# Kernel optimization log

Hardware: AMD Instinct MI355X
Metric: run time of the kernel (lower is better)

## Reference

```python
import jax, jax.numpy as jnp
import numpy as np

N_EXPERTS = 8
D_IN = 1024
D_OUT = 1024
BATCH = 4096


def setup_inputs() -> dict:
    key = jax.random.key(0)
    k_x, k_w, k_b, k_a = jax.random.split(key, 4)
    xs = jax.random.normal(k_x, (BATCH, D_IN), dtype=jnp.float32)
    mxs = jnp.arange(BATCH, dtype=jnp.int32)  # opaque per-sample metadata, passed through
    actions = jax.random.randint(k_a, (BATCH,), 0, N_EXPERTS, dtype=jnp.int64)
    # Expert parameters: each submodule is Linear(D_IN -> D_OUT)
    W = jax.random.normal(k_w, (N_EXPERTS, D_OUT, D_IN), dtype=jnp.float32) / np.sqrt(D_IN)
    b = jax.random.normal(k_b, (N_EXPERTS, D_OUT), dtype=jnp.float32) * 0.01
    return {"xs": xs, "mxs": mxs, "actions": actions, "W": W, "b": b}


def reference(xs, mxs, actions, W, b):
    # Original: per-sample python loop y_i = submodule[actions[i]](x_i); cat along batch.
    # Vectorized: compute all experts densely (E small), then select per-sample row.
    y_all = jnp.einsum("bj,eij->bei", xs, W) + b[None, :, :]  # [B, E, D_OUT]
    ys = jnp.take_along_axis(y_all, actions[:, None, None].astype(jnp.int32), axis=1)
    ys = jnp.squeeze(ys, axis=1)  # [B, D_OUT]
    return (ys, mxs, actions)
```

## Files before the change

kernel.cpp:

```cpp
#include <hip/hip_runtime.h>

#define BATCH 4096
#define D_IN 1024
#define D_OUT 1024
#define N_EXPERTS 8

#define TM 64
#define TN 128
#define TK 32
#define MAX_TILES 71

#define WS_PERM    0
#define WS_STARTS  4096
#define WS_TILE_E  4112
#define WS_TILE_M  4200
#define WS_NTILES  4288

typedef __attribute__((ext_vector_type(8))) short short8;
typedef __attribute__((ext_vector_type(4))) float f32x4;

__global__ void group_kernel(const int* __restrict__ actions, int* __restrict__ ws) {
    __shared__ int cnt[N_EXPERTS];
    __shared__ int base[N_EXPERTS];
    const int t = threadIdx.x;
    if (t < N_EXPERTS) cnt[t] = 0;
    __syncthreads();
    for (int i = t; i < BATCH; i += 256) atomicAdd(&cnt[actions[i]], 1);
    __syncthreads();
    if (t == 0) {
        int s = 0, nt = 0;
        for (int e = 0; e < N_EXPERTS; ++e) {
            const int c = cnt[e];
            base[e] = s;
            ws[WS_STARTS + e] = s;
            for (int m0 = 0; m0 < c; m0 += TM) {
                ws[WS_TILE_E + nt] = e;
                ws[WS_TILE_M + nt] = m0;
                ++nt;
            }
            s += c;
            cnt[e] = 0;
        }
        ws[WS_STARTS + N_EXPERTS] = s;
        ws[WS_NTILES] = nt;
    }
    __syncthreads();
    for (int i = t; i < BATCH; i += 256) {
        const int a = actions[i];
        const int pos = base[a] + atomicAdd(&cnt[a], 1);
        ws[WS_PERM + pos] = i;
    }
}

__device__ __forceinline__ void cvt8(const float4 a, const float4 b,
                                     short8& h, short8& l) {
    float f[8] = {a.x, a.y, a.z, a.w, b.x, b.y, b.z, b.w};
#pragma unroll
    for (int i = 0; i < 8; ++i) {
        const unsigned u = __float_as_uint(f[i]);
        h[i] = (short)(u >> 16);
        const float r = f[i] - __uint_as_float(u & 0xffff0000u);
        l[i] = (short)(__float_as_uint(r) >> 16);
    }
}

__global__ __launch_bounds__(256) void moe_gemm(
    const float* __restrict__ xs, const float* __restrict__ W,
    const float* __restrict__ bias, const int* __restrict__ ws,
    float* __restrict__ out)
{
    const int tix = blockIdx.y;
    if (tix >= ws[WS_NTILES]) return;
    const int e   = ws[WS_TILE_E + tix];
    const int m0  = ws[WS_TILE_M + tix];
    const int s0  = ws[WS_STARTS + e];
    const int cnt = ws[WS_STARTS + e + 1] - s0;
    const int n0  = blockIdx.x * TN;

    __shared__ short Ahi[2][TM * TK];
    __shared__ short Alo[2][TM * TK];
    __shared__ short Bhi[2][TN * TK];
    __shared__ short Blo[2][TN * TK];
    __shared__ int   rows_s[TM];

    const int t = threadIdx.x;
    if (t < TM) {
        const int r = m0 + t;
        rows_s[t] = (r < cnt) ? ws[WS_PERM + s0 + r] : -1;
    }
    __syncthreads();

    const int lane = t & 63;
    const int wave = t >> 6;
    const int wm = (wave & 1) * 32;
    const int wn = (wave >> 1) * 64;

    const float zf = 0.f;
    f32x4 acc[2][4];
#pragma unroll
    for (int mi = 0; mi < 2; ++mi)
#pragma unroll
        for (int nj = 0; nj < 4; ++nj)
            acc[mi][nj] = (f32x4){zf, zf, zf, zf};

    const float* Wb = W + (size_t)e * (D_OUT * (size_t)D_IN) + (size_t)n0 * D_IN;

    const int j  = t & 3;
    const int rr = t >> 2;

    const int arow = rows_s[rr];
    const float* aptr = (arow >= 0) ? (xs + (size_t)arow * D_IN + j * 8) : nullptr;

    const int slotA   = (j * 16 + (rr & 15)) ^ (j << 1);
    const int aoff_st = (rr >> 4) * 512 + slotA * 8;
    const int boff0   = aoff_st;
    const int boff1   = aoff_st + 4 * 512;

    const float* qb0 = Wb + (size_t)rr * D_IN + j * 8;
    const float* qb1 = Wb + (size_t)(64 + rr) * D_IN + j * 8;

    const int rds = (lane ^ ((lane >> 4) << 1)) * 8;

#define LOAD_SET(A0, A1, B0, B1, B2, B3, KOFF) do {                          \
        const int _k = (KOFF);                                               \
        if (aptr) {                                                          \
            A0 = *(const float4*)(aptr + _k);                                \
            A1 = *(const float4*)(aptr + _k + 4);                            \
        }                                                                    \
        B0 = *(const float4*)(qb0 + _k); B1 = *(const float4*)(qb0 + _k + 4);\
        B2 = *(const float4*)(qb1 + _k); B3 = *(const float4*)(qb1 + _k + 4);\
    } while (0)

#define CVT_STORE_SET(A0, A1, B0, B1, B2, B3, BUF) do {                      \
        short8 _h, _l;                                                       \
        cvt8(A0, A1, _h, _l);                                                \
        *(short8*)&Ahi[BUF][aoff_st] = _h; *(short8*)&Alo[BUF][aoff_st] = _l;\
        cvt8(B0, B1, _h, _l);                                                \
        *(short8*)&Bhi[BUF][boff0] = _h;   *(short8*)&Blo[BUF][boff0] = _l;  \
        cvt8(B2, B3, _h, _l);                                                \
        *(short8*)&Bhi[BUF][boff1] = _h;   *(short8*)&Blo[BUF][boff1] = _l;  \
    } while (0)

#define FRAG_MFMA(BUF) do {                                                  \
        short8 ah[2], al[2], bh[4], bl[4];                                   \
        _Pragma("unroll")                                                    \
        for (int i2 = 0; i2 < 2; ++i2) {                                     \
            const int aoff = ((wm >> 4) + i2) * 512 + rds;                   \
            ah[i2] = *(const short8*)&Ahi[BUF][aoff];                        \
            al[i2] = *(const short8*)&Alo[BUF][aoff];                        \
        }                                                                    \
        _Pragma("unroll")                                                    \
        for (int i2 = 0; i2 < 4; ++i2) {                                     \
            const int boff = ((wn >> 4) + i2) * 512 + rds;                   \
            bh[i2] = *(const short8*)&Bhi[BUF][boff];                        \
            bl[i2] = *(const short8*)&Blo[BUF][boff];                        \
        }                                                                    \
        _Pragma("unroll")                                                    \
        for (int mi = 0; mi < 2; ++mi)                                       \
            _Pragma("unroll")                                                \
            for (int nj = 0; nj < 4; ++nj) {                                 \
                acc[mi][nj] = __builtin_amdgcn_mfma_f32_16x16x32_bf16(ah[mi], bh[nj], acc[mi][nj], 0, 0, 0); \
                acc[mi][nj] = __builtin_amdgcn_mfma_f32_16x16x32_bf16(ah[mi], bl[nj], acc[mi][nj], 0, 0, 0); \
                acc[mi][nj] = __builtin_amdgcn_mfma_f32_16x16x32_bf16(al[mi], bh[nj], acc[mi][nj], 0, 0, 0); \
            }                                                                \
    } while (0)

#define PIPE_BARRIER() asm volatile("s_waitcnt lgkmcnt(0)\n\ts_barrier" ::: "memory")

    float4 ax0 = make_float4(0.f, 0.f, 0.f, 0.f), ax1 = ax0;
    float4 bx0, bx1, bx2, bx3;
    float4 ay0 = make_float4(0.f, 0.f, 0.f, 0.f), ay1 = ay0;
    float4 by0, by1, by2, by3;

    LOAD_SET(ax0, ax1, bx0, bx1, bx2, bx3, 0);
    CVT_STORE_SET(ax0, ax1, bx0, bx1, bx2, bx3, 0);
    LOAD_SET(ax0, ax1, bx0, bx1, bx2, bx3, TK);
    PIPE_BARRIER();

    int ke = 2 * TK;
#pragma unroll 1
    for (int i = 0; i < 15; ++i) {
        {
            LOAD_SET(ay0, ay1, by0, by1, by2, by3, ke);
            FRAG_MFMA(0);
            CVT_STORE_SET(ax0, ax1, bx0, bx1, bx2, bx3, 1);
            PIPE_BARRIER();
        }
        {
            LOAD_SET(ax0, ax1, bx0, bx1, bx2, bx3, ke + TK);
            FRAG_MFMA(1);
            CVT_STORE_SET(ay0, ay1, by0, by1, by2, by3, 0);
            PIPE_BARRIER();
        }
        ke += 2 * TK;
    }
    {
        FRAG_MFMA(0);
        CVT_STORE_SET(ax0, ax1, bx0, bx1, bx2, bx3, 1);
        PIPE_BARRIER();
    }
    {
        FRAG_MFMA(1);
    }

#undef LOAD_SET
#undef CVT_STORE_SET
#undef FRAG_MFMA
#undef PIPE_BARRIER

    const int cl = lane & 15;
    const int qd = lane >> 4;
    float bv[4];
#pragma unroll
    for (int nj = 0; nj < 4; ++nj)
        bv[nj] = bias[e * D_OUT + n0 + wn + nj * 16 + cl];
#pragma unroll
    for (int mi = 0; mi < 2; ++mi) {
#pragma unroll
        for (int reg = 0; reg < 4; ++reg) {
            const int mloc = wm + mi * 16 + qd * 4 + reg;
            const int r = rows_s[mloc];
            if (r >= 0) {
                float* orow = out + (size_t)r * D_OUT + n0 + wn + cl;
#pragma unroll
                for (int nj = 0; nj < 4; ++nj)
                    orow[nj * 16] = acc[mi][nj][reg] + bv[nj];
            }
        }
    }
}

__global__ void meta_float_kernel(const int* __restrict__ mxs,
                                  const int* __restrict__ actions,
                                  float* __restrict__ out) {
    const int i = blockIdx.x * 256 + threadIdx.x;
    if (i < BATCH) {
        out[BATCH * D_OUT + i] = (float)mxs[i];
        out[BATCH * D_OUT + BATCH + i] = (float)actions[i];
    }
}

__global__ void meta_raw64_kernel(const int* __restrict__ mxs,
                                  const int* __restrict__ actions,
                                  float* __restrict__ out) {
    const int i = blockIdx.x * 256 + threadIdx.x;
    if (i < BATCH) {
        out[BATCH * D_OUT + i] = (float)mxs[i];
        long long* a64 = (long long*)(out + BATCH * D_OUT + BATCH);
        a64[i] = (long long)actions[i];
    }
}

extern "C" void kernel_launch(void* const* d_in, const int* in_sizes, int n_in,
                              void* d_out, int out_size, void* d_ws, size_t ws_size,
                              hipStream_t stream) {
    const float* xs      = (const float*)d_in[0];
    const int*   mxs     = (const int*)d_in[1];
    const int*   actions = (const int*)d_in[2];
    const float* W       = (const float*)d_in[3];
    const float* bias    = (const float*)d_in[4];
    float* out = (float*)d_out;
    int*   ws  = (int*)d_ws;

    group_kernel<<<1, 256, 0, stream>>>(actions, ws);

    dim3 grid(D_OUT / TN, MAX_TILES, 1);
    moe_gemm<<<grid, 256, 0, stream>>>(xs, W, bias, ws, out);

    const int metaOff = BATCH * D_OUT;
    if (out_size >= metaOff + 3 * BATCH) {
        meta_raw64_kernel<<<(BATCH + 255) / 256, 256, 0, stream>>>(mxs, actions, out);
    } else if (out_size >= metaOff + 2 * BATCH) {
        meta_float_kernel<<<(BATCH + 255) / 256, 256, 0, stream>>>(mxs, actions, out);
    }
}
```

Baseline: 141.7 us.

## Pre-split inputs to bf16 hi/lo in workspace and stream tiles via global_load_lds

A new prep kernel converts all of xs and W into pre-tiled bf16 hi/lo arrays in the workspace. The same kernel also builds the expert grouping with a ballot-based parallel scan and writes the metadata outputs, replacing three separate kernels. The GEMM then loads these pre-converted tiles straight into LDS with global_load_lds, so the main loop no longer does fp32 loads and conversions. The cost is an extra full pass over W and xs every call, plus about 100MB of workspace traffic, with a fallback to the old GEMM when the workspace is too small.

```diff
diff --git a/kernel.cpp b/kernel.cpp
--- a/kernel.cpp
+++ b/kernel.cpp
@@ -16,41 +16,14 @@
 #define WS_TILE_M  4200
 #define WS_NTILES  4288
 
+#define WS_XHI_OFF   32768
+#define WS_XLO_OFF   (32768 + 8388608)
+#define WS_WHI_OFF   (32768 + 2*8388608)
+#define WS_WLO_OFF   (32768 + 2*8388608 + 16777216)
+#define WS_NEEDED    (32768 + 2*8388608 + 2*16777216)
+
 typedef __attribute__((ext_vector_type(8))) short short8;
 typedef __attribute__((ext_vector_type(4))) float f32x4;
-
-__global__ void group_kernel(const int* __restrict__ actions, int* __restrict__ ws) {
-    __shared__ int cnt[N_EXPERTS];
-    __shared__ int base[N_EXPERTS];
-    const int t = threadIdx.x;
-    if (t < N_EXPERTS) cnt[t] = 0;
-    __syncthreads();
-    for (int i = t; i < BATCH; i += 256) atomicAdd(&cnt[actions[i]], 1);
-    __syncthreads();
-    if (t == 0) {
-        int s = 0, nt = 0;
-        for (int e = 0; e < N_EXPERTS; ++e) {
-            const int c = cnt[e];
-            base[e] = s;
-            ws[WS_STARTS + e] = s;
-            for (int m0 = 0; m0 < c; m0 += TM) {
-                ws[WS_TILE_E + nt] = e;
-                ws[WS_TILE_M + nt] = m0;
-                ++nt;
-            }
-            s += c;
-            cnt[e] = 0;
-        }
-        ws[WS_STARTS + N_EXPERTS] = s;
-        ws[WS_NTILES] = nt;
-    }
-    __syncthreads();
-    for (int i = t; i < BATCH; i += 256) {
-        const int a = actions[i];
-        const int pos = base[a] + atomicAdd(&cnt[a], 1);
-        ws[WS_PERM + pos] = i;
-    }
-}
 
 __device__ __forceinline__ void cvt8(const float4 a, const float4 b,
                                      short8& h, short8& l) {
@@ -64,8 +37,148 @@
     }
 }
 
-__global__ __launch_bounds__(256) void moe_gemm(
+__global__ __launch_bounds__(256) void prep_kernel(
+    const int* __restrict__ actions, const int* __restrict__ mxs,
     const float* __restrict__ xs, const float* __restrict__ W,
+    int* __restrict__ ws,
+    short* __restrict__ XhiP, short* __restrict__ XloP,
+    short* __restrict__ WhiP, short* __restrict__ WloP,
+    float* __restrict__ out, int meta_mode)
+{
+    const int bid = blockIdx.x;
+    const int t = threadIdx.x;
+
+    if (bid == 0) {
+        __shared__ int chunkoff[64][N_EXPERTS];
+        const int lane = t & 63;
+        const int wave = t >> 6;
+
+        for (int it = 0; it < 16; ++it) {
+            const int c = wave * 16 + it;
+            const int a = actions[c * 64 + lane];
+            int myc = 0;
+#pragma unroll
+            for (int e = 0; e < N_EXPERTS; ++e) {
+                const unsigned long long me = __ballot(a == e);
+                if (lane == e) myc = (int)__popcll(me);
+            }
+            if (lane < N_EXPERTS) chunkoff[c][lane] = myc;
+        }
+        __syncthreads();
+
+        if (wave == 0) {
+            int cc0 = chunkoff[lane][0], cc1 = chunkoff[lane][1];
+            int cc2 = chunkoff[lane][2], cc3 = chunkoff[lane][3];
+            int cc4 = chunkoff[lane][4], cc5 = chunkoff[lane][5];
+            int cc6 = chunkoff[lane][6], cc7 = chunkoff[lane][7];
+            int tot0, tot1, tot2, tot3, tot4, tot5, tot6, tot7;
+            int ex0, ex1, ex2, ex3, ex4, ex5, ex6, ex7;
+#define SCAN1(CC, TOT, EX) do {                                   \
+            int v = CC;                                           \
+            _Pragma("unroll")                                     \
+            for (int d = 1; d < 64; d <<= 1) {                    \
+                const int u = __shfl_up(v, d, 64);                \
+                if (lane >= d) v += u;                            \
+            }                                                     \
+            TOT = __shfl(v, 63, 64);                              \
+            EX = v - CC;                                          \
+        } while (0)
+            SCAN1(cc0, tot0, ex0); SCAN1(cc1, tot1, ex1);
+            SCAN1(cc2, tot2, ex2); SCAN1(cc3, tot3, ex3);
+            SCAN1(cc4, tot4, ex4); SCAN1(cc5, tot5, ex5);
+            SCAN1(cc6, tot6, ex6); SCAN1(cc7, tot7, ex7);
+#undef SCAN1
+            const int b0 = 0;
+            const int b1 = b0 + tot0, b2 = b1 + tot1, b3 = b2 + tot2;
+            const int b4 = b3 + tot3, b5 = b4 + tot4, b6 = b5 + tot5;
+            const int b7 = b6 + tot6;
+            chunkoff[lane][0] = b0 + ex0; chunkoff[lane][1] = b1 + ex1;
+            chunkoff[lane][2] = b2 + ex2; chunkoff[lane][3] = b3 + ex3;
+            chunkoff[lane][4] = b4 + ex4; chunkoff[lane][5] = b5 + ex5;
+            chunkoff[lane][6] = b6 + ex6; chunkoff[lane][7] = b7 + ex7;
+            if (lane == 0) {
+                ws[WS_STARTS + 0] = b0; ws[WS_STARTS + 1] = b1;
+                ws[WS_STARTS + 2] = b2; ws[WS_STARTS + 3] = b3;
+                ws[WS_STARTS + 4] = b4; ws[WS_STARTS + 5] = b5;
+                ws[WS_STARTS + 6] = b6; ws[WS_STARTS + 7] = b7;
+                ws[WS_STARTS + 8] = BATCH;
+                int nt = 0;
+                int tots[8] = {tot0, tot1, tot2, tot3, tot4, tot5, tot6, tot7};
+#pragma unroll
+                for (int e = 0; e < N_EXPERTS; ++e)
+                    for (int m0 = 0; m0 < tots[e]; m0 += TM) {
+                        ws[WS_TILE_E + nt] = e;
+                        ws[WS_TILE_M + nt] = m0;
+                        ++nt;
+                    }
+                ws[WS_NTILES] = nt;
+            }
+        }
+        __syncthreads();
+
+        for (int it = 0; it < 16; ++it) {
+            const int c = wave * 16 + it;
+            const int i = c * 64 + lane;
+            const int a = actions[i];
+            unsigned long long msel = 0;
+#pragma unroll
+            for (int e = 0; e < N_EXPERTS; ++e) {
+                const unsigned long long me = __ballot(a == e);
+                if (a == e) msel = me;
+            }
+            const int rank = (int)__popcll(msel & ((1ull << lane) - 1ull));
+            const int pos = chunkoff[c][a] + rank;
+            ws[WS_PERM + pos] = i;
+        }
+        return;
+    }
+
+    if (bid <= 16) {
+        const int i = (bid - 1) * 256 + t;
+        if (meta_mode == 2) {
+            out[BATCH * D_OUT + i] = (float)mxs[i];
+            long long* a64 = (long long*)(out + BATCH * D_OUT + BATCH);
+            a64[i] = (long long)actions[i];
+        } else if (meta_mode == 1) {
+            out[BATCH * D_OUT + i] = (float)mxs[i];
+            out[BATCH * D_OUT + BATCH + i] = (float)actions[i];
+        }
+        return;
+    }
+
+    const int g = (bid - 17) * 256 + t;
+    if (g < 1048576) {
+        const int slot = g & 63;
+        const int i2   = (g >> 6) & 7;
+        const int blk  = g >> 9;
+        const int nt   = blk & 7;
+        const int kt   = (blk >> 3) & 31;
+        const int e    = blk >> 8;
+        const int c    = slot & 15;
+        const int j    = slot >> 4;
+        const int n    = nt * 128 + i2 * 16 + c;
+        const float* p = W + ((size_t)(e << 10) + n) * D_IN + kt * 32 + j * 8;
+        const float4 f0 = *(const float4*)p;
+        const float4 f1 = *(const float4*)(p + 4);
+        short8 h, l;
+        cvt8(f0, f1, h, l);
+        *(short8*)(WhiP + (size_t)g * 8) = h;
+        *(short8*)(WloP + (size_t)g * 8) = l;
+    } else {
+        const int g2 = g - 1048576;
+        const float* p = xs + (size_t)g2 * 8;
+        const float4 f0 = *(const float4*)p;
+        const float4 f1 = *(const float4*)(p + 4);
+        short8 h, l;
+        cvt8(f0, f1, h, l);
+        *(short8*)(XhiP + (size_t)g2 * 8) = h;
+        *(short8*)(XloP + (size_t)g2 * 8) = l;
+    }
+}
+
+__global__ __launch_bounds__(256) void moe_gemm_pc(
+    const short* __restrict__ Xhi, const short* __restrict__ Xlo,
+    const short* __restrict__ Whi, const short* __restrict__ Wlo,
     const float* __restrict__ bias, const int* __restrict__ ws,
     float* __restrict__ out)
 {
@@ -77,10 +190,10 @@
     const int cnt = ws[WS_STARTS + e + 1] - s0;
     const int n0  = blockIdx.x * TN;
 
-    __shared__ short Ahi[2][TM * TK];
-    __shared__ short Alo[2][TM * TK];
-    __shared__ short Bhi[2][TN * TK];
-    __shared__ short Blo[2][TN * TK];
+    __shared__ short Ahi[2][4 * 512];
+    __shared__ short Alo[2][4 * 512];
+    __shared__ short Bhi[2][8 * 512];
+    __shared__ short Blo[2][8 * 512];
     __shared__ int   rows_s[TM];
 
     const int t = threadIdx.x;
@@ -88,6 +201,13 @@
         const int r = m0 + t;
         rows_s[t] = (r < cnt) ? ws[WS_PERM + s0 + r] : -1;
     }
+    {
+        const short8 z = {0, 0, 0, 0, 0, 0, 0, 0};
+        ((short8*)&Ahi[0][0])[t] = z;
+        ((short8*)&Ahi[1][0])[t] = z;
+        ((short8*)&Alo[0][0])[t] = z;
+        ((short8*)&Alo[1][0])[t] = z;
+    }
     __syncthreads();
 
     const int lane = t & 63;
@@ -103,43 +223,49 @@
         for (int nj = 0; nj < 4; ++nj)
             acc[mi][nj] = (f32x4){zf, zf, zf, zf};
 
-    const float* Wb = W + (size_t)e * (D_OUT * (size_t)D_IN) + (size_t)n0 * D_IN;
-
-    const int j  = t & 3;
-    const int rr = t >> 2;
-
-    const int arow = rows_s[rr];
-    const float* aptr = (arow >= 0) ? (xs + (size_t)arow * D_IN + j * 8) : nullptr;
-
-    const int slotA   = (j * 16 + (rr & 15)) ^ (j << 1);
-    const int aoff_st = (rr >> 4) * 512 + slotA * 8;
-    const int boff0   = aoff_st;
-    const int boff1   = aoff_st + 4 * 512;
-
-    const float* qb0 = Wb + (size_t)rr * D_IN + j * 8;
-    const float* qb1 = Wb + (size_t)(64 + rr) * D_IN + j * 8;
-
-    const int rds = (lane ^ ((lane >> 4) << 1)) * 8;
-
-#define LOAD_SET(A0, A1, B0, B1, B2, B3, KOFF) do {                          \
-        const int _k = (KOFF);                                               \
-        if (aptr) {                                                          \
-            A0 = *(const float4*)(aptr + _k);                                \
-            A1 = *(const float4*)(aptr + _k + 4);                            \
-        }                                                                    \
-        B0 = *(const float4*)(qb0 + _k); B1 = *(const float4*)(qb0 + _k + 4);\
-        B2 = *(const float4*)(qb1 + _k); B3 = *(const float4*)(qb1 + _k + 4);\
+    const int arow = rows_s[wave * 16 + (lane & 15)];
+    const bool avalid = arow >= 0;
+    const short* aSrcHi = Xhi + (size_t)(avalid ? arow : 0) * D_IN + (lane >> 4) * 8;
+    const short* aSrcLo = Xlo + (size_t)(avalid ? arow : 0) * D_IN + (lane >> 4) * 8;
+
+    const size_t wBase = ((size_t)e * 256 + (size_t)blockIdx.x) * 4096;
+    const size_t bo0 = (size_t)wave * 512 + lane * 8;
+    const size_t bo1 = (size_t)(wave + 4) * 512 + lane * 8;
+
+#define STAGE(KT, BUF) do {                                                    \
+        const int _kt = (KT);                                                  \
+        if (avalid) {                                                          \
+            __builtin_amdgcn_global_load_lds(                                  \
+                (const __attribute__((address_space(1))) void*)(aSrcHi + _kt * 32), \
+                (__attribute__((address_space(3))) void*)&Ahi[BUF][wave * 512],\
+                16, 0, 0);                                                     \
+            __builtin_amdgcn_global_load_lds(                                  \
+                (const __attribute__((address_space(1))) void*)(aSrcLo + _kt * 32), \
+                (__attribute__((address_space(3))) void*)&Alo[BUF][wave * 512],\
+                16, 0, 0);                                                     \
+        }                                                                      \
+        {                                                                      \
+            const size_t _wo = wBase + (size_t)_kt * 32768;                    \
+            __builtin_amdgcn_global_load_lds(                                  \
+                (const __attribute__((address_space(1))) void*)(Whi + _wo + bo0), \
+                (__attribute__((address_space(3))) void*)&Bhi[BUF][wave * 512],\
+                16, 0, 0);                                                     \
+            __builtin_amdgcn_global_load_lds(                                  \
+                (const __attribute__((address_space(1))) void*)(Wlo + _wo + bo0), \
+                (__attribute__((address_space(3))) void*)&Blo[BUF][wave * 512],\
+                16, 0, 0);                                                     \
+            __builtin_amdgcn_global_load_lds(                                  \
+                (const __attribute__((address_space(1))) void*)(Whi + _wo + bo1), \
+                (__attribute__((address_space(3))) void*)&Bhi[BUF][(wave + 4) * 512], \
+                16, 0, 0);                                                     \
+            __builtin_amdgcn_global_load_lds(                                  \
+                (const __attribute__((address_space(1))) void*)(Wlo + _wo + bo1), \
+                (__attribute__((address_space(3))) void*)&Blo[BUF][(wave + 4) * 512], \
+                16, 0, 0);                                                     \
+        }                                                                      \
     } while (0)
 
-#define CVT_STORE_SET(A0, A1, B0, B1, B2, B3, BUF) do {                      \
-        short8 _h, _l;                                                       \
-        cvt8(A0, A1, _h, _l);                                                \
-        *(short8*)&Ahi[BUF][aoff_st] = _h; *(short8*)&Alo[BUF][aoff_st] = _l;\
-        cvt8(B0, B1, _h, _l);                                                \
-        *(short8*)&Bhi[BUF][boff0] = _h;   *(short8*)&Blo[BUF][boff0] = _l;  \
-        cvt8(B2, B3, _h, _l);                                                \
-        *(short8*)&Bhi[BUF][boff1] = _h;   *(short8*)&Blo[BUF][boff1] = _l;  \
-    } while (0)
+    const int rds = lane * 8;
 
 #define FRAG_MFMA(BUF) do {                                                  \
         short8 ah[2], al[2], bh[4], bl[4];                                   \
@@ -165,6 +291,154 @@
             }                                                                \
     } while (0)
 
+#define VBAR() asm volatile("s_waitcnt vmcnt(0) lgkmcnt(0)\n\ts_barrier" ::: "memory")
+
+    STAGE(0, 0);
+    VBAR();
+
+    int kt = 1;
+#pragma unroll 1
+    for (int i = 0; i < 15; ++i) {
+        STAGE(kt, 1);
+        FRAG_MFMA(0);
+        VBAR();
+        STAGE(kt + 1, 0);
+        FRAG_MFMA(1);
+        VBAR();
+        kt += 2;
+    }
+    STAGE(31, 1);
+    FRAG_MFMA(0);
+    VBAR();
+    FRAG_MFMA(1);
+
+#undef STAGE
+#undef FRAG_MFMA
+#undef VBAR
+
+    const int cl = lane & 15;
+    const int qd = lane >> 4;
+    float bv[4];
+#pragma unroll
+    for (int nj = 0; nj < 4; ++nj)
+        bv[nj] = bias[e * D_OUT + n0 + wn + nj * 16 + cl];
+#pragma unroll
+    for (int mi = 0; mi < 2; ++mi) {
+#pragma unroll
+        for (int reg = 0; reg < 4; ++reg) {
+            const int mloc = wm + mi * 16 + qd * 4 + reg;
+            const int r = rows_s[mloc];
+            if (r >= 0) {
+                float* orow = out + (size_t)r * D_OUT + n0 + wn + cl;
+#pragma unroll
+                for (int nj = 0; nj < 4; ++nj)
+                    orow[nj * 16] = acc[mi][nj][reg] + bv[nj];
+            }
+        }
+    }
+}
+
+__global__ __launch_bounds__(256) void moe_gemm_fb(
+    const float* __restrict__ xs, const float* __restrict__ W,
+    const float* __restrict__ bias, const int* __restrict__ ws,
+    float* __restrict__ out)
+{
+    const int tix = blockIdx.y;
+    if (tix >= ws[WS_NTILES]) return;
+    const int e   = ws[WS_TILE_E + tix];
+    const int m0  = ws[WS_TILE_M + tix];
+    const int s0  = ws[WS_STARTS + e];
+    const int cnt = ws[WS_STARTS + e + 1] - s0;
+    const int n0  = blockIdx.x * TN;
+
+    __shared__ short Ahi[2][TM * TK];
+    __shared__ short Alo[2][TM * TK];
+    __shared__ short Bhi[2][TN * TK];
+    __shared__ short Blo[2][TN * TK];
+    __shared__ int   rows_s[TM];
+
+    const int t = threadIdx.x;
+    if (t < TM) {
+        const int r = m0 + t;
+        rows_s[t] = (r < cnt) ? ws[WS_PERM + s0 + r] : -1;
+    }
+    __syncthreads();
+
+    const int lane = t & 63;
+    const int wave = t >> 6;
+    const int wm = (wave & 1) * 32;
+    const int wn = (wave >> 1) * 64;
+
+    const float zf = 0.f;
+    f32x4 acc[2][4];
+#pragma unroll
+    for (int mi = 0; mi < 2; ++mi)
+#pragma unroll
+        for (int nj = 0; nj < 4; ++nj)
+            acc[mi][nj] = (f32x4){zf, zf, zf, zf};
+
+    const float* Wb = W + (size_t)e * (D_OUT * (size_t)D_IN) + (size_t)n0 * D_IN;
+
+    const int j  = t & 3;
+    const int rr = t >> 2;
+
+    const int arow = rows_s[rr];
+    const float* aptr = (arow >= 0) ? (xs + (size_t)arow * D_IN + j * 8) : nullptr;
+
+    const int slotA   = (j * 16 + (rr & 15)) ^ (j << 1);
+    const int aoff_st = (rr >> 4) * 512 + slotA * 8;
+    const int boff0   = aoff_st;
+    const int boff1   = aoff_st + 4 * 512;
+
+    const float* qb0 = Wb + (size_t)rr * D_IN + j * 8;
+    const float* qb1 = Wb + (size_t)(64 + rr) * D_IN + j * 8;
+
+    const int rds = (lane ^ ((lane >> 4) << 1)) * 8;
+
+#define LOAD_SET(A0, A1, B0, B1, B2, B3, KOFF) do {                          \
+        const int _k = (KOFF);                                               \
+        if (aptr) {                                                          \
+            A0 = *(const float4*)(aptr + _k);                                \
+            A1 = *(const float4*)(aptr + _k + 4);                            \
+        }                                                                    \
+        B0 = *(const float4*)(qb0 + _k); B1 = *(const float4*)(qb0 + _k + 4);\
+        B2 = *(const float4*)(qb1 + _k); B3 = *(const float4*)(qb1 + _k + 4);\
+    } while (0)
+
+#define CVT_STORE_SET(A0, A1, B0, B1, B2, B3, BUF) do {                      \
+        short8 _h, _l;                                                       \
+        cvt8(A0, A1, _h, _l);                                                \
+        *(short8*)&Ahi[BUF][aoff_st] = _h; *(short8*)&Alo[BUF][aoff_st] = _l;\
+        cvt8(B0, B1, _h, _l);                                                \
+        *(short8*)&Bhi[BUF][boff0] = _h;   *(short8*)&Blo[BUF][boff0] = _l;  \
+        cvt8(B2, B3, _h, _l);                                                \
+        *(short8*)&Bhi[BUF][boff1] = _h;   *(short8*)&Blo[BUF][boff1] = _l;  \
+    } while (0)
+
+#define FRAG_MFMA(BUF) do {                                                  \
+        short8 ah[2], al[2], bh[4], bl[4];                                   \
+        _Pragma("unroll")                                                    \
+        for (int i2 = 0; i2 < 2; ++i2) {                                     \
+            const int aoff = ((wm >> 4) + i2) * 512 + rds;                   \
+            ah[i2] = *(const short8*)&Ahi[BUF][aoff];                        \
+            al[i2] = *(const short8*)&Alo[BUF][aoff];                        \
+        }                                                                    \
+        _Pragma("unroll")                                                    \
+        for (int i2 = 0; i2 < 4; ++i2) {                                     \
+            const int boff = ((wn >> 4) + i2) * 512 + rds;                   \
+            bh[i2] = *(const short8*)&Bhi[BUF][boff];                        \
+            bl[i2] = *(const short8*)&Blo[BUF][boff];                        \
+        }                                                                    \
+        _Pragma("unroll")                                                    \
+        for (int mi = 0; mi < 2; ++mi)                                       \
+            _Pragma("unroll")                                                \
+            for (int nj = 0; nj < 4; ++nj) {                                 \
+                acc[mi][nj] = __builtin_amdgcn_mfma_f32_16x16x32_bf16(ah[mi], bh[nj], acc[mi][nj], 0, 0, 0); \
+                acc[mi][nj] = __builtin_amdgcn_mfma_f32_16x16x32_bf16(ah[mi], bl[nj], acc[mi][nj], 0, 0, 0); \
+                acc[mi][nj] = __builtin_amdgcn_mfma_f32_16x16x32_bf16(al[mi], bh[nj], acc[mi][nj], 0, 0, 0); \
+            }                                                                \
+    } while (0)
+
 #define PIPE_BARRIER() asm volatile("s_waitcnt lgkmcnt(0)\n\ts_barrier" ::: "memory")
 
     float4 ax0 = make_float4(0.f, 0.f, 0.f, 0.f), ax1 = ax0;
@@ -227,27 +501,6 @@
                     orow[nj * 16] = acc[mi][nj][reg] + bv[nj];
             }
         }
-    }
-}
-
-__global__ void meta_float_kernel(const int* __restrict__ mxs,
-                                  const int* __restrict__ actions,
-                                  float* __restrict__ out) {
-    const int i = blockIdx.x * 256 + threadIdx.x;
-    if (i < BATCH) {
-        out[BATCH * D_OUT + i] = (float)mxs[i];
-        out[BATCH * D_OUT + BATCH + i] = (float)actions[i];
-    }
-}
-
-__global__ void meta_raw64_kernel(const int* __restrict__ mxs,
-                                  const int* __restrict__ actions,
-                                  float* __restrict__ out) {
-    const int i = blockIdx.x * 256 + threadIdx.x;
-    if (i < BATCH) {
-        out[BATCH * D_OUT + i] = (float)mxs[i];
-        long long* a64 = (long long*)(out + BATCH * D_OUT + BATCH);
-        a64[i] = (long long)actions[i];
     }
 }
 
@@ -261,16 +514,27 @@
     const float* bias    = (const float*)d_in[4];
     float* out = (float*)d_out;
     int*   ws  = (int*)d_ws;
-
-    group_kernel<<<1, 256, 0, stream>>>(actions, ws);
+    char*  wsb = (char*)d_ws;
+
+    short* XhiP = (short*)(wsb + WS_XHI_OFF);
+    short* XloP = (short*)(wsb + WS_XLO_OFF);
+    short* WhiP = (short*)(wsb + WS_WHI_OFF);
+    short* WloP = (short*)(wsb + WS_WLO_OFF);
+
+    const int metaOff = BATCH * D_OUT;
+    const int meta_mode = (out_size >= metaOff + 3 * BATCH) ? 2
+                        : (out_size >= metaOff + 2 * BATCH) ? 1 : 0;
+
+    const bool big = ws_size >= (size_t)WS_NEEDED;
+    const int prep_blocks = big ? (17 + 6144) : 17;
+
+    prep_kernel<<<prep_blocks, 256, 0, stream>>>(
+        actions, mxs, xs, W, ws, XhiP, XloP, WhiP, WloP, out, meta_mode);
 
     dim3 grid(D_OUT / TN, MAX_TILES, 1);
-    moe_gemm<<<grid, 256, 0, stream>>>(xs, W, bias, ws, out);
-
-    const int metaOff = BATCH * D_OUT;
-    if (out_size >= metaOff + 3 * BATCH) {
-        meta_raw64_kernel<<<(BATCH + 255) / 256, 256, 0, stream>>>(mxs, actions, out);
-    } else if (out_size >= metaOff + 2 * BATCH) {
-        meta_float_kernel<<<(BATCH + 255) / 256, 256, 0, stream>>>(mxs, actions, out);
+    if (big) {
+        moe_gemm_pc<<<grid, 256, 0, stream>>>(XhiP, XloP, WhiP, WloP, bias, ws, out);
+    } else {
+        moe_gemm_fb<<<grid, 256, 0, stream>>>(xs, W, bias, ws, out);
     }
 }
```

Result: slower. 153.7 us (+8.4%).

## Enlarge MoE GEMM tiles to 128x128, fuse grouping with metadata kernel

Applied to the files above, without the earlier changes.

Raises the GEMM row tile from 64 to 128 with 512 threads (8 waves), so each block reuses each W tile across twice as many tokens. This halves redundant weight traffic and the fp32-to-bf16 split conversion of W per row tile. It also rewrites the grouping kernel to use wave ballots and prefix-scans instead of shared atomics and a serial loop, and folds the metadata copy into the same launch to save a kernel launch. The larger tiles waste more padding rows at expert boundaries and give fewer blocks for occupancy.

```diff
diff --git a/kernel.cpp b/kernel.cpp
--- a/kernel.cpp
+++ b/kernel.cpp
@@ -5,52 +5,19 @@
 #define D_OUT 1024
 #define N_EXPERTS 8
 
-#define TM 64
-#define TN 128
 #define TK 32
-#define MAX_TILES 71
+#define TMX 128
+#define TNX 128
+#define MAX_TILES_128 39
 
 #define WS_PERM    0
 #define WS_STARTS  4096
 #define WS_TILE_E  4112
-#define WS_TILE_M  4200
-#define WS_NTILES  4288
+#define WS_TILE_M  4160
+#define WS_NTILES  4208
 
 typedef __attribute__((ext_vector_type(8))) short short8;
 typedef __attribute__((ext_vector_type(4))) float f32x4;
-
-__global__ void group_kernel(const int* __restrict__ actions, int* __restrict__ ws) {
-    __shared__ int cnt[N_EXPERTS];
-    __shared__ int base[N_EXPERTS];
-    const int t = threadIdx.x;
-    if (t < N_EXPERTS) cnt[t] = 0;
-    __syncthreads();
-    for (int i = t; i < BATCH; i += 256) atomicAdd(&cnt[actions[i]], 1);
-    __syncthreads();
-    if (t == 0) {
-        int s = 0, nt = 0;
-        for (int e = 0; e < N_EXPERTS; ++e) {
-            const int c = cnt[e];
-            base[e] = s;
-            ws[WS_STARTS + e] = s;
-            for (int m0 = 0; m0 < c; m0 += TM) {
-                ws[WS_TILE_E + nt] = e;
-                ws[WS_TILE_M + nt] = m0;
-                ++nt;
-            }
-            s += c;
-            cnt[e] = 0;
-        }
-        ws[WS_STARTS + N_EXPERTS] = s;
-        ws[WS_NTILES] = nt;
-    }
-    __syncthreads();
-    for (int i = t; i < BATCH; i += 256) {
-        const int a = actions[i];
-        const int pos = base[a] + atomicAdd(&cnt[a], 1);
-        ws[WS_PERM + pos] = i;
-    }
-}
 
 __device__ __forceinline__ void cvt8(const float4 a, const float4 b,
                                      short8& h, short8& l) {
@@ -64,7 +31,110 @@
     }
 }
 
-__global__ __launch_bounds__(256) void moe_gemm(
+__global__ __launch_bounds__(256) void group_meta_kernel(
+    const int* __restrict__ actions, const int* __restrict__ mxs,
+    int* __restrict__ ws, float* __restrict__ out, int meta_mode)
+{
+    const int bid = blockIdx.x;
+    const int t = threadIdx.x;
+
+    if (bid == 0) {
+        __shared__ int chunkoff[64][N_EXPERTS];
+        const int lane = t & 63;
+        const int wave = t >> 6;
+
+        for (int it = 0; it < 16; ++it) {
+            const int c = wave * 16 + it;
+            const int a = actions[c * 64 + lane];
+            int myc = 0;
+#pragma unroll
+            for (int e = 0; e < N_EXPERTS; ++e) {
+                const unsigned long long me = __ballot(a == e);
+                if (lane == e) myc = (int)__popcll(me);
+            }
+            if (lane < N_EXPERTS) chunkoff[c][lane] = myc;
+        }
+        __syncthreads();
+
+        if (wave == 0) {
+            int cc0 = chunkoff[lane][0], cc1 = chunkoff[lane][1];
+            int cc2 = chunkoff[lane][2], cc3 = chunkoff[lane][3];
+            int cc4 = chunkoff[lane][4], cc5 = chunkoff[lane][5];
+            int cc6 = chunkoff[lane][6], cc7 = chunkoff[lane][7];
+            int tot0, tot1, tot2, tot3, tot4, tot5, tot6, tot7;
+            int ex0, ex1, ex2, ex3, ex4, ex5, ex6, ex7;
+#define SCAN1(CC, TOT, EX) do {                                   \
+            int v = CC;                                           \
+            _Pragma("unroll")                                     \
+            for (int d = 1; d < 64; d <<= 1) {                    \
+                const int u = __shfl_up(v, d, 64);                \
+                if (lane >= d) v += u;                            \
+            }                                                     \
+            TOT = __shfl(v, 63, 64);                              \
+            EX = v - CC;                                          \
+        } while (0)
+            SCAN1(cc0, tot0, ex0); SCAN1(cc1, tot1, ex1);
+            SCAN1(cc2, tot2, ex2); SCAN1(cc3, tot3, ex3);
+            SCAN1(cc4, tot4, ex4); SCAN1(cc5, tot5, ex5);
+            SCAN1(cc6, tot6, ex6); SCAN1(cc7, tot7, ex7);
+#undef SCAN1
+            const int b0 = 0;
+            const int b1 = b0 + tot0, b2 = b1 + tot1, b3 = b2 + tot2;
+            const int b4 = b3 + tot3, b5 = b4 + tot4, b6 = b5 + tot5;
+            const int b7 = b6 + tot6;
+            chunkoff[lane][0] = b0 + ex0; chunkoff[lane][1] = b1 + ex1;
+            chunkoff[lane][2] = b2 + ex2; chunkoff[lane][3] = b3 + ex3;
+            chunkoff[lane][4] = b4 + ex4; chunkoff[lane][5] = b5 + ex5;
+            chunkoff[lane][6] = b6 + ex6; chunkoff[lane][7] = b7 + ex7;
+            if (lane == 0) {
+                ws[WS_STARTS + 0] = b0; ws[WS_STARTS + 1] = b1;
+                ws[WS_STARTS + 2] = b2; ws[WS_STARTS + 3] = b3;
+                ws[WS_STARTS + 4] = b4; ws[WS_STARTS + 5] = b5;
+                ws[WS_STARTS + 6] = b6; ws[WS_STARTS + 7] = b7;
+                ws[WS_STARTS + 8] = BATCH;
+                int nt = 0;
+                int tots[8] = {tot0, tot1, tot2, tot3, tot4, tot5, tot6, tot7};
+#pragma unroll
+                for (int e = 0; e < N_EXPERTS; ++e)
+                    for (int m0 = 0; m0 < tots[e]; m0 += TMX) {
+                        ws[WS_TILE_E + nt] = e;
+                        ws[WS_TILE_M + nt] = m0;
+                        ++nt;
+                    }
+                ws[WS_NTILES] = nt;
+            }
+        }
+        __syncthreads();
+
+        for (int it = 0; it < 16; ++it) {
+            const int c = wave * 16 + it;
+            const int i = c * 64 + lane;
+            const int a = actions[i];
+            unsigned long long msel = 0;
+#pragma unroll
+            for (int e = 0; e < N_EXPERTS; ++e) {
+                const unsigned long long me = __ballot(a == e);
+                if (a == e) msel = me;
+            }
+            const int rank = (int)__popcll(msel & ((1ull << lane) - 1ull));
+            const int pos = chunkoff[c][a] + rank;
+            ws[WS_PERM + pos] = i;
+        }
+        return;
+    }
+
+    const int i = (bid - 1) * 256 + t;
+    if (meta_mode == 2) {
+        out[BATCH * D_OUT + i] = (float)mxs[i];
+        long long* a64 = (long long*)(out + BATCH * D_OUT + BATCH);
+        a64[i] = (long long)actions[i];
+    } else if (meta_mode == 1) {
+        out[BATCH * D_OUT + i] = (float)mxs[i];
+        out[BATCH * D_OUT + BATCH + i] = (float)actions[i];
+    }
+}
+
+__global__ __launch_bounds__(512) void moe_gemm(
     const float* __restrict__ xs, const float* __restrict__ W,
     const float* __restrict__ bias, const int* __restrict__ ws,
     float* __restrict__ out)
@@ -75,16 +145,16 @@
     const int m0  = ws[WS_TILE_M + tix];
     const int s0  = ws[WS_STARTS + e];
     const int cnt = ws[WS_STARTS + e + 1] - s0;
-    const int n0  = blockIdx.x * TN;
-
-    __shared__ short Ahi[2][TM * TK];
-    __shared__ short Alo[2][TM * TK];
-    __shared__ short Bhi[2][TN * TK];
-    __shared__ short Blo[2][TN * TK];
-    __shared__ int   rows_s[TM];
+    const int n0  = blockIdx.x * TNX;
+
+    __shared__ short Ahi[2][8 * 512];
+    __shared__ short Alo[2][8 * 512];
+    __shared__ short Bhi[2][8 * 512];
+    __shared__ short Blo[2][8 * 512];
+    __shared__ int   rows_s[TMX];
 
     const int t = threadIdx.x;
-    if (t < TM) {
+    if (t < TMX) {
         const int r = m0 + t;
         rows_s[t] = (r < cnt) ? ws[WS_PERM + s0 + r] : -1;
     }
@@ -92,8 +162,8 @@
 
     const int lane = t & 63;
     const int wave = t >> 6;
-    const int wm = (wave & 1) * 32;
-    const int wn = (wave >> 1) * 64;
+    const int wm = (wave >> 1) * 32;
+    const int wn = (wave & 1) * 64;
 
     const float zf = 0.f;
     f32x4 acc[2][4];
@@ -111,34 +181,28 @@
     const int arow = rows_s[rr];
     const float* aptr = (arow >= 0) ? (xs + (size_t)arow * D_IN + j * 8) : nullptr;
 
-    const int slotA   = (j * 16 + (rr & 15)) ^ (j << 1);
-    const int aoff_st = (rr >> 4) * 512 + slotA * 8;
-    const int boff0   = aoff_st;
-    const int boff1   = aoff_st + 4 * 512;
-
-    const float* qb0 = Wb + (size_t)rr * D_IN + j * 8;
-    const float* qb1 = Wb + (size_t)(64 + rr) * D_IN + j * 8;
+    const int slotS  = (j * 16 + (rr & 15)) ^ (j << 1);
+    const int off_st = (rr >> 4) * 512 + slotS * 8;
+
+    const float* qb = Wb + (size_t)rr * D_IN + j * 8;
 
     const int rds = (lane ^ ((lane >> 4) << 1)) * 8;
 
-#define LOAD_SET(A0, A1, B0, B1, B2, B3, KOFF) do {                          \
+#define LOAD_SET(A0, A1, B0, B1, KOFF) do {                                  \
         const int _k = (KOFF);                                               \
         if (aptr) {                                                          \
             A0 = *(const float4*)(aptr + _k);                                \
             A1 = *(const float4*)(aptr + _k + 4);                            \
         }                                                                    \
-        B0 = *(const float4*)(qb0 + _k); B1 = *(const float4*)(qb0 + _k + 4);\
-        B2 = *(const float4*)(qb1 + _k); B3 = *(const float4*)(qb1 + _k + 4);\
+        B0 = *(const float4*)(qb + _k); B1 = *(const float4*)(qb + _k + 4);  \
     } while (0)
 
-#define CVT_STORE_SET(A0, A1, B0, B1, B2, B3, BUF) do {                      \
+#define CVT_STORE_SET(A0, A1, B0, B1, BUF) do {                              \
         short8 _h, _l;                                                       \
         cvt8(A0, A1, _h, _l);                                                \
-        *(short8*)&Ahi[BUF][aoff_st] = _h; *(short8*)&Alo[BUF][aoff_st] = _l;\
+        *(short8*)&Ahi[BUF][off_st] = _h; *(short8*)&Alo[BUF][off_st] = _l;  \
         cvt8(B0, B1, _h, _l);                                                \
-        *(short8*)&Bhi[BUF][boff0] = _h;   *(short8*)&Blo[BUF][boff0] = _l;  \
-        cvt8(B2, B3, _h, _l);                                                \
-        *(short8*)&Bhi[BUF][boff1] = _h;   *(short8*)&Blo[BUF][boff1] = _l;  \
+        *(short8*)&Bhi[BUF][off_st] = _h; *(short8*)&Blo[BUF][off_st] = _l;  \
     } while (0)
 
 #define FRAG_MFMA(BUF) do {                                                  \
@@ -168,35 +232,35 @@
 #define PIPE_BARRIER() asm volatile("s_waitcnt lgkmcnt(0)\n\ts_barrier" ::: "memory")
 
     float4 ax0 = make_float4(0.f, 0.f, 0.f, 0.f), ax1 = ax0;
-    float4 bx0, bx1, bx2, bx3;
+    float4 bx0, bx1;
     float4 ay0 = make_float4(0.f, 0.f, 0.f, 0.f), ay1 = ay0;
-    float4 by0, by1, by2, by3;
-
-    LOAD_SET(ax0, ax1, bx0, bx1, bx2, bx3, 0);
-    CVT_STORE_SET(ax0, ax1, bx0, bx1, bx2, bx3, 0);
-    LOAD_SET(ax0, ax1, bx0, bx1, bx2, bx3, TK);
+    float4 by0, by1;
+
+    LOAD_SET(ax0, ax1, bx0, bx1, 0);
+    CVT_STORE_SET(ax0, ax1, bx0, bx1, 0);
+    LOAD_SET(ax0, ax1, bx0, bx1, TK);
     PIPE_BARRIER();
 
     int ke = 2 * TK;
 #pragma unroll 1
     for (int i = 0; i < 15; ++i) {
         {
-            LOAD_SET(ay0, ay1, by0, by1, by2, by3, ke);
+            LOAD_SET(ay0, ay1, by0, by1, ke);
             FRAG_MFMA(0);
-            CVT_STORE_SET(ax0, ax1, bx0, bx1, bx2, bx3, 1);
+            CVT_STORE_SET(ax0, ax1, bx0, bx1, 1);
             PIPE_BARRIER();
         }
         {
-            LOAD_SET(ax0, ax1, bx0, bx1, bx2, bx3, ke + TK);
+            LOAD_SET(ax0, ax1, bx0, bx1, ke + TK);
             FRAG_MFMA(1);
-            CVT_STORE_SET(ay0, ay1, by0, by1, by2, by3, 0);
+            CVT_STORE_SET(ay0, ay1, by0, by1, 0);
             PIPE_BARRIER();
         }
         ke += 2 * TK;
     }
     {
         FRAG_MFMA(0);
-        CVT_STORE_SET(ax0, ax1, bx0, bx1, bx2, bx3, 1);
+        CVT_STORE_SET(ax0, ax1, bx0, bx1, 1);
         PIPE_BARRIER();
     }
     {
@@ -227,27 +291,6 @@
                     orow[nj * 16] = acc[mi][nj][reg] + bv[nj];
             }
         }
-    }
-}
-
-__global__ void meta_float_kernel(const int* __restrict__ mxs,
-                                  const int* __restrict__ actions,
-                                  float* __restrict__ out) {
-    const int i = blockIdx.x * 256 + threadIdx.x;
-    if (i < BATCH) {
-        out[BATCH * D_OUT + i] = (float)mxs[i];
-        out[BATCH * D_OUT + BATCH + i] = (float)actions[i];
-    }
-}
-
-__global__ void meta_raw64_kernel(const int* __restrict__ mxs,
-                                  const int* __restrict__ actions,
-                                  float* __restrict__ out) {
-    const int i = blockIdx.x * 256 + threadIdx.x;
-    if (i < BATCH) {
-        out[BATCH * D_OUT + i] = (float)mxs[i];
-        long long* a64 = (long long*)(out + BATCH * D_OUT + BATCH);
-        a64[i] = (long long)actions[i];
     }
 }
 
@@ -262,15 +305,12 @@
     float* out = (float*)d_out;
     int*   ws  = (int*)d_ws;
 
-    group_kernel<<<1, 256, 0, stream>>>(actions, ws);
-
-    dim3 grid(D_OUT / TN, MAX_TILES, 1);
-    moe_gemm<<<grid, 256, 0, stream>>>(xs, W, bias, ws, out);
-
     const int metaOff = BATCH * D_OUT;
-    if (out_size >= metaOff + 3 * BATCH) {
-        meta_raw64_kernel<<<(BATCH + 255) / 256, 256, 0, stream>>>(mxs, actions, out);
-    } else if (out_size >= metaOff + 2 * BATCH) {
-        meta_float_kernel<<<(BATCH + 255) / 256, 256, 0, stream>>>(mxs, actions, out);
-    }
+    const int meta_mode = (out_size >= metaOff + 3 * BATCH) ? 2
+                        : (out_size >= metaOff + 2 * BATCH) ? 1 : 0;
+
+    group_meta_kernel<<<17, 256, 0, stream>>>(actions, mxs, ws, out, meta_mode);
+
+    dim3 grid(D_OUT / TNX, MAX_TILES_128, 1);
+    moe_gemm<<<grid, 512, 0, stream>>>(xs, W, bias, ws, out);
 }
```

Result: no change. 141.2 us (-0.3%).
